# Kernel optimization log

Hardware: AMD Instinct MI355X
Metric: run time of the kernel (lower is better)

Reference implementation:

```python
import jax, jax.numpy as jnp
import numpy as np

S, B, H, NL = 2048, 32, 1024, 2


def setup_inputs() -> dict:
    key = jax.random.key(0)
    k1, k2, k3, k4, k5 = jax.random.split(key, 5)
    hidden = jax.random.normal(k1, (NL, B, H), dtype=jnp.float32)
    encoder_outputs = jax.random.normal(k2, (S, B, H), dtype=jnp.float32)
    # nn.Linear(2H, H): weight [H, 2H], bias [H]
    attn_w = jax.random.normal(k3, (H, 2 * H), dtype=jnp.float32) / np.sqrt(2.0 * H)
    attn_b = jax.random.normal(k4, (H,), dtype=jnp.float32) * 0.01
    # v ~ N(0, 1/sqrt(H))
    v = jax.random.normal(k5, (H,), dtype=jnp.float32) / np.sqrt(H)
    return {"hidden": hidden, "encoder_outputs": encoder_outputs,
            "attn_w": attn_w, "attn_b": attn_b, "v": v}


def reference(hidden, encoder_outputs, attn_w, attn_b, v):
    # hidden: [NL, B, H]; encoder_outputs: [S, B, H]
    max_len = encoder_outputs.shape[0]
    h = jnp.broadcast_to(hidden[-1], (max_len,) + hidden[-1].shape)  # [S, B, H]
    x = jnp.concatenate([h, encoder_outputs], axis=2)                 # [S, B, 2H]
    energy = jnp.tanh(jnp.einsum('sbk,hk->sbh', x, attn_w) + attn_b)  # [S, B, H]
    scores = jnp.einsum('sbh,h->bs', energy, v)                       # [B, S]
    return jax.nn.softmax(scores, axis=1)
```

## Files before the change

kernel.cpp:

```cpp
#include <hip/hip_runtime.h>
#include <stdint.h>


#define S_LEN 2048
#define B_SZ 32
#define H_SZ 1024
#define M_TOT (S_LEN * B_SZ)
#define K_TOT H_SZ
#define NCB 8
#define BK 64
#define TILE_SHORTS 8192

typedef __attribute__((ext_vector_type(8))) short short8;
typedef __attribute__((ext_vector_type(4))) float f32x4;

static __device__ __forceinline__ unsigned short f2bf(float x) {
  uint32_t u = __builtin_bit_cast(uint32_t, x);
  u += 0x7FFFu + ((u >> 16) & 1u);
  return (unsigned short)(u >> 16);
}
static __device__ __forceinline__ uint32_t pack2(float a, float b) {
  return (uint32_t)f2bf(a) | ((uint32_t)f2bf(b) << 16);
}
static __device__ __forceinline__ float fast_tanh(float x) {
  float e = __expf(2.0f * x);
  return 1.0f - 2.0f / (e + 1.0f);
}

__global__ void __launch_bounds__(256) prep_u_kernel(
    const float* __restrict__ hidden, const float* __restrict__ attn_w,
    const float* __restrict__ attn_b, float* __restrict__ u) {
  __shared__ float hs[4][H_SZ];
  const int hc = blockIdx.x;
  const int bg = blockIdx.y;
  const int tid = threadIdx.x;
  for (int i = tid; i < 4 * H_SZ; i += 256) {
    const int bi = i >> 10, k = i & 1023;
    hs[bi][k] = hidden[(size_t)B_SZ * H_SZ + (size_t)(bg * 4 + bi) * H_SZ + k];
  }
  __syncthreads();
  const int h = hc * 256 + tid;
  const float* wrow = attn_w + (size_t)h * (2 * H_SZ);
  float s0 = 0.f, s1 = 0.f, s2 = 0.f, s3 = 0.f;
#pragma unroll 4
  for (int k = 0; k < H_SZ; k += 4) {
    float4 w4 = *reinterpret_cast<const float4*>(wrow + k);
    s0 += w4.x * hs[0][k] + w4.y * hs[0][k + 1] + w4.z * hs[0][k + 2] + w4.w * hs[0][k + 3];
    s1 += w4.x * hs[1][k] + w4.y * hs[1][k + 1] + w4.z * hs[1][k + 2] + w4.w * hs[1][k + 3];
    s2 += w4.x * hs[2][k] + w4.y * hs[2][k + 1] + w4.z * hs[2][k + 2] + w4.w * hs[2][k + 3];
    s3 += w4.x * hs[3][k] + w4.y * hs[3][k + 1] + w4.z * hs[3][k + 2] + w4.w * hs[3][k + 3];
  }
  const float bb = attn_b[h];
  u[(size_t)(bg * 4 + 0) * H_SZ + h] = s0 + bb;
  u[(size_t)(bg * 4 + 1) * H_SZ + h] = s1 + bb;
  u[(size_t)(bg * 4 + 2) * H_SZ + h] = s2 + bb;
  u[(size_t)(bg * 4 + 3) * H_SZ + h] = s3 + bb;
}

__global__ void __launch_bounds__(256) prep_a_kernel(
    const float* __restrict__ enc, unsigned short* __restrict__ Aimg) {
  const int idx = blockIdx.x * 256 + threadIdx.x;
  const int m = idx >> 7, sl = idx & 127;
  const int kb = sl >> 3, s8 = sl & 7;
  const float4* src =
      reinterpret_cast<const float4*>(enc + (size_t)m * K_TOT + kb * BK + s8 * 8);
  float4 f0 = src[0], f1 = src[1];
  uint4 o;
  o.x = pack2(f0.x, f0.y); o.y = pack2(f0.z, f0.w);
  o.z = pack2(f1.x, f1.y); o.w = pack2(f1.z, f1.w);
  const int row = m & 127;
  const size_t tile = (size_t)(m >> 7) * 16 + kb;
  unsigned short* dst = Aimg + tile * TILE_SHORTS + row * 64 + ((s8 ^ (row & 7)) << 3);
  *reinterpret_cast<uint4*>(dst) = o;
}

__global__ void __launch_bounds__(256) prep_b_kernel(
    const float* __restrict__ attn_w, unsigned short* __restrict__ Bimg) {
  const int idx = blockIdx.x * 256 + threadIdx.x;
  const int n = idx >> 7, sl = idx & 127;
  const int kb = sl >> 3, s8 = sl & 7;
  const float4* src = reinterpret_cast<const float4*>(
      attn_w + (size_t)n * 2048 + 1024 + kb * BK + s8 * 8);
  float4 f0 = src[0], f1 = src[1];
  uint4 o;
  o.x = pack2(f0.x, f0.y); o.y = pack2(f0.z, f0.w);
  o.z = pack2(f1.x, f1.y); o.w = pack2(f1.z, f1.w);
  const int row = n & 127;
  const size_t tile = (size_t)(n >> 7) * 16 + kb;
  unsigned short* dst = Bimg + tile * TILE_SHORTS + row * 64 + ((s8 ^ (row & 7)) << 3);
  *reinterpret_cast<uint4*>(dst) = o;
}

#define LGKM0  asm volatile("s_waitcnt lgkmcnt(0)" ::: "memory")
#define VM0    asm volatile("s_waitcnt vmcnt(0)" ::: "memory")
#define VMCNT8 asm volatile("s_waitcnt vmcnt(8)" ::: "memory")
#define BARRIER __builtin_amdgcn_s_barrier()

__global__ void __launch_bounds__(256, 2) gemm_img_kernel(
    const unsigned short* __restrict__ Aimg, const unsigned short* __restrict__ Bimg,
    const float* __restrict__ u, const float* __restrict__ v,
    float* __restrict__ pscore) {
  __shared__ unsigned short As[2][TILE_SHORTS];
  __shared__ unsigned short Bs[2][TILE_SHORTS];
  __shared__ float rowsum[2][128];

  const int tid = threadIdx.x;
  const int wid = tid >> 6, lane = tid & 63;
  const int wr = wid >> 1, wc = wid & 1;

  const int wg = blockIdx.x;
  const int xcd = wg & 7, li = wg >> 3;
  const int rp = xcd * 64 + (li >> 3);
  const int cb = li & 7;
  const int brow = rp * 128, bcol = cb * 128;

  const unsigned short* Ag = Aimg + (size_t)rp * 16 * TILE_SHORTS;
  const unsigned short* Bg = Bimg + (size_t)cb * 16 * TILE_SHORTS;

  f32x4 acc[4][4];
#pragma unroll
  for (int i = 0; i < 4; ++i)
#pragma unroll
    for (int j = 0; j < 4; ++j) acc[i][j] = (f32x4){0.f, 0.f, 0.f, 0.f};

  const int fr = lane & 15, g = lane >> 4;
  const int soff0 = ((g) ^ (fr & 7)) << 3;
  const int soff1 = ((4 + g) ^ (fr & 7)) << 3;
  const int arow_base = (wr * 64 + fr) * 64;
  const int brow_base = (wc * 64 + fr) * 64;
  const int stg = wid * 2048;

#define STAGE(BUF, KB)                                                          \
  do {                                                                          \
    const unsigned short* at_ = Ag + (KB) * TILE_SHORTS + stg + lane * 8;       \
    const unsigned short* bt_ = Bg + (KB) * TILE_SHORTS + stg + lane * 8;       \
    _Pragma("unroll")                                                           \
    for (int j_ = 0; j_ < 4; ++j_) {                                            \
      __builtin_amdgcn_global_load_lds(                                         \
          (const __attribute__((address_space(1))) void*)(at_ + j_ * 512),      \
          (__attribute__((address_space(3))) void*)(&As[BUF][stg + j_ * 512]),  \
          16, 0, 0);                                                            \
      __builtin_amdgcn_global_load_lds(                                         \
          (const __attribute__((address_space(1))) void*)(bt_ + j_ * 512),      \
          (__attribute__((address_space(3))) void*)(&Bs[BUF][stg + j_ * 512]),  \
          16, 0, 0);                                                            \
    }                                                                           \
  } while (0)

#define COMPUTE(BUF)                                                            \
  do {                                                                          \
    short8 af[4], bf[4];                                                        \
    _Pragma("unroll")                                                           \
    for (int i_ = 0; i_ < 4; ++i_)                                              \
      af[i_] = *reinterpret_cast<const short8*>(                                \
          &As[BUF][arow_base + i_ * 1024 + soff0]);                             \
    _Pragma("unroll")                                                           \
    for (int j_ = 0; j_ < 4; ++j_)                                              \
      bf[j_] = *reinterpret_cast<const short8*>(                                \
          &Bs[BUF][brow_base + j_ * 1024 + soff0]);                             \
    _Pragma("unroll")                                                           \
    for (int i_ = 0; i_ < 4; ++i_)                                              \
      _Pragma("unroll")                                                         \
      for (int j_ = 0; j_ < 4; ++j_)                                            \
        acc[i_][j_] = __builtin_amdgcn_mfma_f32_16x16x32_bf16(                  \
            af[i_], bf[j_], acc[i_][j_], 0, 0, 0);                              \
    _Pragma("unroll")                                                           \
    for (int i_ = 0; i_ < 4; ++i_)                                              \
      af[i_] = *reinterpret_cast<const short8*>(                                \
          &As[BUF][arow_base + i_ * 1024 + soff1]);                             \
    _Pragma("unroll")                                                           \
    for (int j_ = 0; j_ < 4; ++j_)                                              \
      bf[j_] = *reinterpret_cast<const short8*>(                                \
          &Bs[BUF][brow_base + j_ * 1024 + soff1]);                             \
    _Pragma("unroll")                                                           \
    for (int i_ = 0; i_ < 4; ++i_)                                              \
      _Pragma("unroll")                                                         \
      for (int j_ = 0; j_ < 4; ++j_)                                            \
        acc[i_][j_] = __builtin_amdgcn_mfma_f32_16x16x32_bf16(                  \
            af[i_], bf[j_], acc[i_][j_], 0, 0, 0);                              \
  } while (0)

  STAGE(0, 0);
  STAGE(1, 1);
  int cur = 0;
#pragma unroll 1
  for (int t = 0; t < 16; ++t) {
    if (t < 15) { VMCNT8; } else { VM0; }
    BARRIER;
    if (cur == 0) COMPUTE(0); else COMPUTE(1);
    LGKM0;
    BARRIER;
    if (t + 2 < 16) {
      if (cur == 0) STAGE(0, t + 2); else STAGE(1, t + 2);
    }
    cur ^= 1;
  }
#undef STAGE
#undef COMPUTE

  float vv[4];
#pragma unroll
  for (int j = 0; j < 4; ++j) vv[j] = v[bcol + wc * 64 + j * 16 + fr];

  const int g4 = g * 4;
#pragma unroll
  for (int i = 0; i < 4; ++i) {
#pragma unroll
    for (int reg = 0; reg < 4; ++reg) {
      const int rloc = wr * 64 + i * 16 + g4 + reg;
      const int bb = (brow + rloc) & (B_SZ - 1);
      float rs = 0.f;
#pragma unroll
      for (int j = 0; j < 4; ++j) {
        const int h = bcol + wc * 64 + j * 16 + fr;
        float val = acc[i][j][reg] + u[(size_t)bb * H_SZ + h];
        rs += vv[j] * fast_tanh(val);
      }
      rs += __shfl_xor(rs, 1);
      rs += __shfl_xor(rs, 2);
      rs += __shfl_xor(rs, 4);
      rs += __shfl_xor(rs, 8);
      if (fr == 0) rowsum[wc][rloc] = rs;
    }
  }
  __syncthreads();
  if (tid < 128)
    pscore[(size_t)cb * M_TOT + brow + tid] = rowsum[0][tid] + rowsum[1][tid];
}

__global__ void __launch_bounds__(256) prep_w2_flat_kernel(
    const float* __restrict__ attn_w, unsigned short* __restrict__ Bt) {
  const int idx = blockIdx.x * 256 + threadIdx.x;
  const int base = idx * 4;
  const int n = base >> 10, k = base & 1023;
  float4 w = *reinterpret_cast<const float4*>(attn_w + (size_t)n * 2048 + 1024 + k);
  ushort4 o;
  o.x = f2bf(w.x); o.y = f2bf(w.y); o.z = f2bf(w.z); o.w = f2bf(w.w);
  *reinterpret_cast<ushort4*>(Bt + base) = o;
}

__global__ void __launch_bounds__(256) gemm_fused_kernel(
    const float* __restrict__ A, const unsigned short* __restrict__ Bt,
    const float* __restrict__ u, const float* __restrict__ v,
    float* __restrict__ pscore) {
  __shared__ unsigned short As[128 * 32];
  __shared__ unsigned short Bs[128 * 32];
  __shared__ float rowsum[2][128];
  const int tid = threadIdx.x;
  const int wid = tid >> 6, lane = tid & 63;
  const int wr = wid >> 1, wc = wid & 1;
  const int cb = blockIdx.x;
  const int brow = blockIdx.y * 128;
  const int bcol = cb * 128;
  const int arow_st = tid >> 1;
  const int acol_st = (tid & 1) * 16;
  const float* Ag = A + (size_t)(brow + arow_st) * K_TOT + acol_st;
  unsigned short* AsW = As + arow_st * 32 + acol_st;
  const int chunk0 = wid * 2;
  const unsigned short* Bg0 =
      Bt + (size_t)(bcol + chunk0 * 16 + (lane >> 2)) * K_TOT + (lane & 3) * 8;
  f32x4 acc[4][4];
#pragma unroll
  for (int i = 0; i < 4; ++i)
#pragma unroll
    for (int j = 0; j < 4; ++j) acc[i][j] = (f32x4){0.f, 0.f, 0.f, 0.f};
  const int fr = lane & 15;
  const int kseg = (lane >> 4) * 8;
  for (int k0 = 0; k0 < K_TOT; k0 += 32) {
    __syncthreads();
    const float4* ap = reinterpret_cast<const float4*>(Ag + k0);
    float4 f0 = ap[0], f1 = ap[1], f2 = ap[2], f3 = ap[3];
    uint4 w0, w1;
    w0.x = pack2(f0.x, f0.y); w0.y = pack2(f0.z, f0.w);
    w0.z = pack2(f1.x, f1.y); w0.w = pack2(f1.z, f1.w);
    w1.x = pack2(f2.x, f2.y); w1.y = pack2(f2.z, f2.w);
    w1.z = pack2(f3.x, f3.y); w1.w = pack2(f3.z, f3.w);
    *reinterpret_cast<uint4*>(AsW) = w0;
    *reinterpret_cast<uint4*>(AsW + 8) = w1;
    __builtin_amdgcn_global_load_lds(
        (const __attribute__((address_space(1))) void*)(Bg0 + k0),
        (__attribute__((address_space(3))) void*)(Bs + chunk0 * 512), 16, 0, 0);
    __builtin_amdgcn_global_load_lds(
        (const __attribute__((address_space(1))) void*)(Bg0 + 16 * K_TOT + k0),
        (__attribute__((address_space(3))) void*)(Bs + chunk0 * 512 + 512), 16, 0, 0);
    __syncthreads();
    short8 af[4], bf[4];
#pragma unroll
    for (int i = 0; i < 4; ++i)
      af[i] = *reinterpret_cast<const short8*>(As + (wr * 64 + i * 16 + fr) * 32 + kseg);
#pragma unroll
    for (int j = 0; j < 4; ++j)
      bf[j] = *reinterpret_cast<const short8*>(Bs + (wc * 64 + j * 16 + fr) * 32 + kseg);
#pragma unroll
    for (int i = 0; i < 4; ++i)
#pragma unroll
      for (int j = 0; j < 4; ++j)
        acc[i][j] = __builtin_amdgcn_mfma_f32_16x16x32_bf16(af[i], bf[j], acc[i][j], 0, 0, 0);
  }
  float vv[4];
#pragma unroll
  for (int j = 0; j < 4; ++j) vv[j] = v[bcol + wc * 64 + j * 16 + fr];
  const int g4 = (lane >> 4) * 4;
#pragma unroll
  for (int i = 0; i < 4; ++i) {
#pragma unroll
    for (int reg = 0; reg < 4; ++reg) {
      const int rloc = wr * 64 + i * 16 + g4 + reg;
      const int bb = (brow + rloc) & (B_SZ - 1);
      float rs = 0.f;
#pragma unroll
      for (int j = 0; j < 4; ++j) {
        const int h = bcol + wc * 64 + j * 16 + fr;
        float val = acc[i][j][reg] + u[(size_t)bb * H_SZ + h];
        rs += vv[j] * fast_tanh(val);
      }
      rs += __shfl_xor(rs, 1);
      rs += __shfl_xor(rs, 2);
      rs += __shfl_xor(rs, 4);
      rs += __shfl_xor(rs, 8);
      if (fr == 0) rowsum[wc][rloc] = rs;
    }
  }
  __syncthreads();
  if (tid < 128)
    pscore[(size_t)cb * M_TOT + brow + tid] = rowsum[0][tid] + rowsum[1][tid];
}

__global__ void __launch_bounds__(256) softmax_kernel(
    const float* __restrict__ ps, float* __restrict__ out) {
  const int b = blockIdx.x, tid = threadIdx.x;
  const int wid = tid >> 6, lane = tid & 63;
  __shared__ float sred[4];
  float vals[8];
  float mx = -1e30f;
#pragma unroll
  for (int ii = 0; ii < 8; ++ii) {
    const int s = ii * 256 + tid;
    float sum = 0.f;
#pragma unroll
    for (int cbk = 0; cbk < NCB; ++cbk) sum += ps[(size_t)cbk * M_TOT + s * B_SZ + b];
    vals[ii] = sum;
    mx = fmaxf(mx, sum);
  }
#pragma unroll
  for (int m = 1; m < 64; m <<= 1) mx = fmaxf(mx, __shfl_xor(mx, m));
  if (lane == 0) sred[wid] = mx;
  __syncthreads();
  mx = fmaxf(fmaxf(sred[0], sred[1]), fmaxf(sred[2], sred[3]));
  __syncthreads();
  float es = 0.f;
#pragma unroll
  for (int ii = 0; ii < 8; ++ii) {
    vals[ii] = __expf(vals[ii] - mx);
    es += vals[ii];
  }
#pragma unroll
  for (int m = 1; m < 64; m <<= 1) es += __shfl_xor(es, m);
  if (lane == 0) sred[wid] = es;
  __syncthreads();
  es = sred[0] + sred[1] + sred[2] + sred[3];
  const float inv = 1.0f / es;
#pragma unroll
  for (int ii = 0; ii < 8; ++ii) out[(size_t)b * S_LEN + ii * 256 + tid] = vals[ii] * inv;
}

extern "C" void kernel_launch(void* const* d_in, const int* in_sizes, int n_in,
                              void* d_out, int out_size, void* d_ws, size_t ws_size,
                              hipStream_t stream) {
  const float* hidden = (const float*)d_in[0];
  const float* enc    = (const float*)d_in[1];
  const float* attn_w = (const float*)d_in[2];
  const float* attn_b = (const float*)d_in[3];
  const float* v      = (const float*)d_in[4];
  float* out = (float*)d_out;

  const size_t A_BYTES = (size_t)M_TOT * K_TOT * 2;
  const size_t B_BYTES = (size_t)K_TOT * K_TOT * 2;
  const size_t U_BYTES = (size_t)B_SZ * H_SZ * 4;
  const size_t P_BYTES = (size_t)NCB * M_TOT * 4;
  char* w = (char*)d_ws;

  if (ws_size >= A_BYTES + B_BYTES + U_BYTES + P_BYTES) {
    unsigned short* Aimg = (unsigned short*)w;
    unsigned short* Bimg = (unsigned short*)(w + A_BYTES);
    float* u  = (float*)(w + A_BYTES + B_BYTES);
    float* ps = (float*)(w + A_BYTES + B_BYTES + U_BYTES);
    prep_u_kernel<<<dim3(4, 8), 256, 0, stream>>>(hidden, attn_w, attn_b, u);
    prep_b_kernel<<<512, 256, 0, stream>>>(attn_w, Bimg);
    prep_a_kernel<<<M_TOT * 128 / 256, 256, 0, stream>>>(enc, Aimg);
    gemm_img_kernel<<<NCB * (M_TOT / 128), 256, 0, stream>>>(Aimg, Bimg, u, v, ps);
    softmax_kernel<<<B_SZ, 256, 0, stream>>>(ps, out);
  } else {
    unsigned short* Bt = (unsigned short*)w;
    float* u  = (float*)(w + B_BYTES);
    float* ps = (float*)(w + B_BYTES + U_BYTES);
    prep_u_kernel<<<dim3(4, 8), 256, 0, stream>>>(hidden, attn_w, attn_b, u);
    prep_w2_flat_kernel<<<1024, 256, 0, stream>>>(attn_w, Bt);
    gemm_fused_kernel<<<dim3(NCB, M_TOT / 128), 256, 0, stream>>>(enc, Bt, u, v, ps);
    softmax_kernel<<<B_SZ, 256, 0, stream>>>(ps, out);
  }
}
```

Before: 369.2 us.

## Enlarge GEMM block tile to 256x256 with 8 waves per block

Raises the main bf16 MFMA GEMM block tile from 128x128 to 256x256, with 512 threads (8 waves in a 2x4 grid, each computing 128x64). The A/B image layouts, staging, and the rowsum/pscore epilogue are rescaled to match, so there are half as many column blocks to reduce in softmax. The intent is more data reuse per byte of global/LDS traffic and less redundant A reads. In exchange it uses 128 KB of LDS per block at the declared 2 blocks per CU, doubles accumulator registers per wave, and launches far fewer workgroups.

```diff
diff --git a/kernel.cpp b/kernel.cpp
--- a/kernel.cpp
+++ b/kernel.cpp
@@ -7,9 +7,9 @@
 #define H_SZ 1024
 #define M_TOT (S_LEN * B_SZ)
 #define K_TOT H_SZ
-#define NCB 8
+#define NCB 4
 #define BK 64
-#define TILE_SHORTS 8192
+#define TS 16384
 
 typedef __attribute__((ext_vector_type(8))) short short8;
 typedef __attribute__((ext_vector_type(4))) float f32x4;
@@ -68,9 +68,9 @@
   uint4 o;
   o.x = pack2(f0.x, f0.y); o.y = pack2(f0.z, f0.w);
   o.z = pack2(f1.x, f1.y); o.w = pack2(f1.z, f1.w);
-  const int row = m & 127;
-  const size_t tile = (size_t)(m >> 7) * 16 + kb;
-  unsigned short* dst = Aimg + tile * TILE_SHORTS + row * 64 + ((s8 ^ (row & 7)) << 3);
+  const int row = m & 255;
+  const size_t tile = (size_t)(m >> 8) * 16 + kb;
+  unsigned short* dst = Aimg + tile * TS + row * 64 + ((s8 ^ (row & 7)) << 3);
   *reinterpret_cast<uint4*>(dst) = o;
 }
 
@@ -85,9 +85,9 @@
   uint4 o;
   o.x = pack2(f0.x, f0.y); o.y = pack2(f0.z, f0.w);
   o.z = pack2(f1.x, f1.y); o.w = pack2(f1.z, f1.w);
-  const int row = n & 127;
-  const size_t tile = (size_t)(n >> 7) * 16 + kb;
-  unsigned short* dst = Bimg + tile * TILE_SHORTS + row * 64 + ((s8 ^ (row & 7)) << 3);
+  const int row = n & 255;
+  const size_t tile = (size_t)(n >> 8) * 16 + kb;
+  unsigned short* dst = Bimg + tile * TS + row * 64 + ((s8 ^ (row & 7)) << 3);
   *reinterpret_cast<uint4*>(dst) = o;
 }
 
@@ -96,88 +96,85 @@
 #define VMCNT8 asm volatile("s_waitcnt vmcnt(8)" ::: "memory")
 #define BARRIER __builtin_amdgcn_s_barrier()
 
-__global__ void __launch_bounds__(256, 2) gemm_img_kernel(
+__global__ void __launch_bounds__(512, 2) gemm_img_kernel(
     const unsigned short* __restrict__ Aimg, const unsigned short* __restrict__ Bimg,
     const float* __restrict__ u, const float* __restrict__ v,
     float* __restrict__ pscore) {
-  __shared__ unsigned short As[2][TILE_SHORTS];
-  __shared__ unsigned short Bs[2][TILE_SHORTS];
-  __shared__ float rowsum[2][128];
+  __shared__ unsigned short As[2][TS];
+  __shared__ unsigned short Bs[2][TS];
+  __shared__ float rowsum[4][256];
 
   const int tid = threadIdx.x;
   const int wid = tid >> 6, lane = tid & 63;
-  const int wr = wid >> 1, wc = wid & 1;
+  const int wr = wid >> 2, wc = wid & 3;
 
   const int wg = blockIdx.x;
   const int xcd = wg & 7, li = wg >> 3;
-  const int rp = xcd * 64 + (li >> 3);
-  const int cb = li & 7;
-  const int brow = rp * 128, bcol = cb * 128;
-
-  const unsigned short* Ag = Aimg + (size_t)rp * 16 * TILE_SHORTS;
-  const unsigned short* Bg = Bimg + (size_t)cb * 16 * TILE_SHORTS;
-
-  f32x4 acc[4][4];
-#pragma unroll
-  for (int i = 0; i < 4; ++i)
+  const int rp = xcd * 32 + (li >> 2);
+  const int cb = li & 3;
+  const int brow = rp * 256, bcol = cb * 256;
+
+  const unsigned short* Ag = Aimg + (size_t)rp * 16 * TS;
+  const unsigned short* Bg = Bimg + (size_t)cb * 16 * TS;
+
+  f32x4 acc[8][4];
+#pragma unroll
+  for (int i = 0; i < 8; ++i)
 #pragma unroll
     for (int j = 0; j < 4; ++j) acc[i][j] = (f32x4){0.f, 0.f, 0.f, 0.f};
 
   const int fr = lane & 15, g = lane >> 4;
   const int soff0 = ((g) ^ (fr & 7)) << 3;
   const int soff1 = ((4 + g) ^ (fr & 7)) << 3;
-  const int arow_base = (wr * 64 + fr) * 64;
+  const int arow_base = (wr * 128 + fr) * 64;
   const int brow_base = (wc * 64 + fr) * 64;
-  const int stg = wid * 2048;
+  const int stg = wid * 512;
 
 #define STAGE(BUF, KB)                                                          \
   do {                                                                          \
-    const unsigned short* at_ = Ag + (KB) * TILE_SHORTS + stg + lane * 8;       \
-    const unsigned short* bt_ = Bg + (KB) * TILE_SHORTS + stg + lane * 8;       \
+    const unsigned short* at_ = Ag + (KB) * TS + stg + lane * 8;                \
+    const unsigned short* bt_ = Bg + (KB) * TS + stg + lane * 8;                \
     _Pragma("unroll")                                                           \
     for (int j_ = 0; j_ < 4; ++j_) {                                            \
       __builtin_amdgcn_global_load_lds(                                         \
-          (const __attribute__((address_space(1))) void*)(at_ + j_ * 512),      \
-          (__attribute__((address_space(3))) void*)(&As[BUF][stg + j_ * 512]),  \
+          (const __attribute__((address_space(1))) void*)(at_ + j_ * 4096),     \
+          (__attribute__((address_space(3))) void*)(&As[BUF][stg + j_ * 4096]), \
           16, 0, 0);                                                            \
       __builtin_amdgcn_global_load_lds(                                         \
-          (const __attribute__((address_space(1))) void*)(bt_ + j_ * 512),      \
-          (__attribute__((address_space(3))) void*)(&Bs[BUF][stg + j_ * 512]),  \
+          (const __attribute__((address_space(1))) void*)(bt_ + j_ * 4096),     \
+          (__attribute__((address_space(3))) void*)(&Bs[BUF][stg + j_ * 4096]), \
           16, 0, 0);                                                            \
     }                                                                           \
   } while (0)
 
 #define COMPUTE(BUF)                                                            \
   do {                                                                          \
-    short8 af[4], bf[4];                                                        \
+    short8 bf0[4], bf1[4];                                                      \
     _Pragma("unroll")                                                           \
-    for (int i_ = 0; i_ < 4; ++i_)                                              \
-      af[i_] = *reinterpret_cast<const short8*>(                                \
-          &As[BUF][arow_base + i_ * 1024 + soff0]);                             \
+    for (int n_ = 0; n_ < 4; ++n_) {                                            \
+      bf0[n_] = *reinterpret_cast<const short8*>(                               \
+          &Bs[BUF][brow_base + n_ * 1024 + soff0]);                             \
+      bf1[n_] = *reinterpret_cast<const short8*>(                               \
+          &Bs[BUF][brow_base + n_ * 1024 + soff1]);                             \
+    }                                                                           \
     _Pragma("unroll")                                                           \
-    for (int j_ = 0; j_ < 4; ++j_)                                              \
-      bf[j_] = *reinterpret_cast<const short8*>(                                \
-          &Bs[BUF][brow_base + j_ * 1024 + soff0]);                             \
+    for (int m_ = 0; m_ < 8; ++m_) {                                            \
+      short8 a0 = *reinterpret_cast<const short8*>(                             \
+          &As[BUF][arow_base + m_ * 1024 + soff0]);                             \
+      _Pragma("unroll")                                                         \
+      for (int n_ = 0; n_ < 4; ++n_)                                            \
+        acc[m_][n_] = __builtin_amdgcn_mfma_f32_16x16x32_bf16(                  \
+            a0, bf0[n_], acc[m_][n_], 0, 0, 0);                                 \
+    }                                                                           \
     _Pragma("unroll")                                                           \
-    for (int i_ = 0; i_ < 4; ++i_)                                              \
+    for (int m_ = 0; m_ < 8; ++m_) {                                            \
+      short8 a1 = *reinterpret_cast<const short8*>(                             \
+          &As[BUF][arow_base + m_ * 1024 + soff1]);                             \
       _Pragma("unroll")                                                         \
-      for (int j_ = 0; j_ < 4; ++j_)                                            \
-        acc[i_][j_] = __builtin_amdgcn_mfma_f32_16x16x32_bf16(                  \
-            af[i_], bf[j_], acc[i_][j_], 0, 0, 0);                              \
-    _Pragma("unroll")                                                           \
-    for (int i_ = 0; i_ < 4; ++i_)                                              \
-      af[i_] = *reinterpret_cast<const short8*>(                                \
-          &As[BUF][arow_base + i_ * 1024 + soff1]);                             \
-    _Pragma("unroll")                                                           \
-    for (int j_ = 0; j_ < 4; ++j_)                                              \
-      bf[j_] = *reinterpret_cast<const short8*>(                                \
-          &Bs[BUF][brow_base + j_ * 1024 + soff1]);                             \
-    _Pragma("unroll")                                                           \
-    for (int i_ = 0; i_ < 4; ++i_)                                              \
-      _Pragma("unroll")                                                         \
-      for (int j_ = 0; j_ < 4; ++j_)                                            \
-        acc[i_][j_] = __builtin_amdgcn_mfma_f32_16x16x32_bf16(                  \
-            af[i_], bf[j_], acc[i_][j_], 0, 0, 0);                              \
+      for (int n_ = 0; n_ < 4; ++n_)                                            \
+        acc[m_][n_] = __builtin_amdgcn_mfma_f32_16x16x32_bf16(                  \
+            a1, bf1[n_], acc[m_][n_], 0, 0, 0);                                 \
+    }                                                                           \
   } while (0)
 
   STAGE(0, 0);
@@ -204,10 +201,10 @@
 
   const int g4 = g * 4;
 #pragma unroll
-  for (int i = 0; i < 4; ++i) {
+  for (int i = 0; i < 8; ++i) {
 #pragma unroll
     for (int reg = 0; reg < 4; ++reg) {
-      const int rloc = wr * 64 + i * 16 + g4 + reg;
+      const int rloc = wr * 128 + i * 16 + g4 + reg;
       const int bb = (brow + rloc) & (B_SZ - 1);
       float rs = 0.f;
 #pragma unroll
@@ -224,8 +221,9 @@
     }
   }
   __syncthreads();
-  if (tid < 128)
-    pscore[(size_t)cb * M_TOT + brow + tid] = rowsum[0][tid] + rowsum[1][tid];
+  if (tid < 256)
+    pscore[(size_t)cb * M_TOT + brow + tid] =
+        rowsum[0][tid] + rowsum[1][tid] + rowsum[2][tid] + rowsum[3][tid];
 }
 
 __global__ void __launch_bounds__(256) prep_w2_flat_kernel(
@@ -327,7 +325,7 @@
 }
 
 __global__ void __launch_bounds__(256) softmax_kernel(
-    const float* __restrict__ ps, float* __restrict__ out) {
+    const float* __restrict__ ps, float* __restrict__ out, int ncb) {
   const int b = blockIdx.x, tid = threadIdx.x;
   const int wid = tid >> 6, lane = tid & 63;
   __shared__ float sred[4];
@@ -337,8 +335,7 @@
   for (int ii = 0; ii < 8; ++ii) {
     const int s = ii * 256 + tid;
     float sum = 0.f;
-#pragma unroll
-    for (int cbk = 0; cbk < NCB; ++cbk) sum += ps[(size_t)cbk * M_TOT + s * B_SZ + b];
+    for (int cbk = 0; cbk < ncb; ++cbk) sum += ps[(size_t)cbk * M_TOT + s * B_SZ + b];
     vals[ii] = sum;
     mx = fmaxf(mx, sum);
   }
@@ -377,7 +374,7 @@
   const size_t A_BYTES = (size_t)M_TOT * K_TOT * 2;
   const size_t B_BYTES = (size_t)K_TOT * K_TOT * 2;
   const size_t U_BYTES = (size_t)B_SZ * H_SZ * 4;
-  const size_t P_BYTES = (size_t)NCB * M_TOT * 4;
+  const size_t P_BYTES = (size_t)8 * M_TOT * 4;
   char* w = (char*)d_ws;
 
   if (ws_size >= A_BYTES + B_BYTES + U_BYTES + P_BYTES) {
@@ -388,15 +385,15 @@
     prep_u_kernel<<<dim3(4, 8), 256, 0, stream>>>(hidden, attn_w, attn_b, u);
     prep_b_kernel<<<512, 256, 0, stream>>>(attn_w, Bimg);
     prep_a_kernel<<<M_TOT * 128 / 256, 256, 0, stream>>>(enc, Aimg);
-    gemm_img_kernel<<<NCB * (M_TOT / 128), 256, 0, stream>>>(Aimg, Bimg, u, v, ps);
-    softmax_kernel<<<B_SZ, 256, 0, stream>>>(ps, out);
+    gemm_img_kernel<<<NCB * (M_TOT / 256), 512, 0, stream>>>(Aimg, Bimg, u, v, ps);
+    softmax_kernel<<<B_SZ, 256, 0, stream>>>(ps, out, NCB);
   } else {
     unsigned short* Bt = (unsigned short*)w;
     float* u  = (float*)(w + B_BYTES);
     float* ps = (float*)(w + B_BYTES + U_BYTES);
     prep_u_kernel<<<dim3(4, 8), 256, 0, stream>>>(hidden, attn_w, attn_b, u);
     prep_w2_flat_kernel<<<1024, 256, 0, stream>>>(attn_w, Bt);
-    gemm_fused_kernel<<<dim3(NCB, M_TOT / 128), 256, 0, stream>>>(enc, Bt, u, v, ps);
-    softmax_kernel<<<B_SZ, 256, 0, stream>>>(ps, out);
-  }
-}
+    gemm_fused_kernel<<<dim3(8, M_TOT / 128), 256, 0, stream>>>(enc, Bt, u, v, ps);
+    softmax_kernel<<<B_SZ, 256, 0, stream>>>(ps, out, 8);
+  }
+}
```

Measured after the change: 593.2 us. 1.61x slower.
